# Kernel tuning notes

Hardware: AMD Instinct MI355X
Metric: run time of the kernel (lower is better)

The kernel has to match this reference:

```python
import jax, jax.numpy as jnp
import numpy as np

T, B, E, H = 512, 128, 512, 512
MEM, CTX = 500, 300

def setup_inputs() -> dict:
    key = jax.random.key(0)
    ks = jax.random.split(key, 16)
    s = 0.05
    return {
        "input_seqs": jax.random.normal(ks[0], (B, T, E), jnp.float32),
        "input_lengths": jax.random.randint(ks[1], (B,), 1, T + 1),
        "Wih_f": jax.random.normal(ks[2], (4 * H, E + CTX), jnp.float32) * s,
        "Whh_f": jax.random.normal(ks[3], (4 * H, H), jnp.float32) * s,
        "bih_f": jax.random.normal(ks[4], (4 * H,), jnp.float32) * s,
        "bhh_f": jax.random.normal(ks[5], (4 * H,), jnp.float32) * s,
        "Wih_b": jax.random.normal(ks[6], (4 * H, E + CTX), jnp.float32) * s,
        "Whh_b": jax.random.normal(ks[7], (4 * H, H), jnp.float32) * s,
        "bih_b": jax.random.normal(ks[8], (4 * H,), jnp.float32) * s,
        "bhh_b": jax.random.normal(ks[9], (4 * H,), jnp.float32) * s,
        "Mk_f": jax.random.normal(ks[10], (MEM, H), jnp.float32) * s,
        "Mv_f": jax.random.normal(ks[11], (CTX, MEM), jnp.float32) * s,
        "Mk_b": jax.random.normal(ks[12], (MEM, H), jnp.float32) * s,
        "Mv_b": jax.random.normal(ks[13], (CTX, MEM), jnp.float32) * s,
    }

def _mem_ctx(h, Mk, Mv):
    # exp-key softmax read: exp(h Mk^T) normalized by row sum, then project to CTX
    a = jnp.exp(h @ Mk.T)                      # [B, MEM]
    return (a / jnp.sum(a, axis=-1, keepdims=True)) @ Mv.T  # [B, CTX]

def _cell(x, h, c, Wih, Whh, b):
    g = x @ Wih.T + h @ Whh.T + b              # [B, 4H], gate order i,f,g,o
    i, f, gg, o = jnp.split(g, 4, axis=-1)
    c = jax.nn.sigmoid(f) * c + jax.nn.sigmoid(i) * jnp.tanh(gg)
    return jax.nn.sigmoid(o) * jnp.tanh(c), c

def reference(input_seqs, input_lengths, Wih_f, Whh_f, bih_f, bhh_f,
              Wih_b, Whh_b, bih_b, bhh_b, Mk_f, Mv_f, Mk_b, Mv_b):
    xs = jnp.transpose(input_seqs, (1, 0, 2))          # [T, B, E]
    dt = xs.dtype
    mask = (jnp.arange(T)[:, None] < input_lengths[None, :]).astype(dt)[:, :, None]  # [T,B,1]
    b_f = bih_f + bhh_f
    b_b = bih_b + bhh_b
    z = jnp.zeros((B, H), dt)
    zf = jnp.zeros((), dt)
    one = jnp.ones((), dt)

    def fstep(carry, x):
        h, c, flag = carry
        ctx = flag * _mem_ctx(h, Mk_f, Mv_f)           # step 0 uses zero dummy context
        h, c = _cell(jnp.concatenate([x, ctx], -1), h, c, Wih_f, Whh_f, b_f)
        return (h, c, one), h
    _, f_hs = jax.lax.scan(fstep, (z, z, zf), xs)      # [T, B, H] per-step hidden

    def bstep(carry, xm):
        x, m = xm
        hm, h, c, flag = carry
        ctx = flag * _mem_ctx(hm, Mk_b, Mv_b)
        h, c = _cell(jnp.concatenate([x, ctx], -1), h, c, Wih_b, Whh_b, b_b)
        return (h * m, h, c, one), None                # masked hidden feeds next memory read
    (h_b, _, _, _), _ = jax.lax.scan(bstep, (z, z, z, zf), (xs[::-1], mask[::-1]))

    idx = jnp.clip(input_lengths - 1, 0, T - 1)
    h_f = f_hs[idx, jnp.arange(B)]                     # final valid forward hidden per example
    # permute(1,2,0).view(B,-1): interleave fwd/bwd per hidden unit
    return jnp.stack([h_f, h_b], axis=-1).reshape(B, 2 * H)
```

## Files before the change

### kernel.cpp

```cpp
#include <hip/hip_runtime.h>
#include <hip/hip_bf16.h>

#define T_   512
#define B_   128
#define E_   512
#define H_   512
#define G4_  2048
#define MEM_ 500
#define CTX_ 300
#define EC_  (E_ + CTX_)
#define SPIN_MAX 65536

typedef short sh8  __attribute__((ext_vector_type(8)));
typedef float f32x4 __attribute__((ext_vector_type(4)));

struct ScanParams {
  const float* __restrict__ x;
  const short* __restrict__ xbf;
  const int*   __restrict__ len;
  const float* __restrict__ Wih0; const float* __restrict__ Whh0;
  const float* __restrict__ bih0; const float* __restrict__ bhh0;
  const float* __restrict__ Wih1; const float* __restrict__ Whh1;
  const float* __restrict__ bih1; const float* __restrict__ bhh1;
  const float* __restrict__ Mk0;  const float* __restrict__ Mk1;
  const float* __restrict__ Mf;
  short* __restrict__ hbf;
  short* __restrict__ aB;
  unsigned* __restrict__ bar;
  float* __restrict__ out;
};

__device__ __forceinline__ float sigm_(float x) { return 1.f / (1.f + __expf(-x)); }
__device__ __forceinline__ float tanh_(float x) { return 1.f - 2.f / (__expf(2.f * x) + 1.f); }
__device__ __forceinline__ short f2bs(float f) {
  __hip_bfloat16 h = __float2bfloat16(f);
  short s; __builtin_memcpy(&s, &h, 2); return s;
}
__device__ __forceinline__ float bs2f(short s) {
  unsigned u = ((unsigned)(unsigned short)s) << 16;
  float f; __builtin_memcpy(&f, &u, 4); return f;
}

struct F16 { sh8 v[16]; };
__device__ __forceinline__ void gld16(F16& f, const short* base) {
  asm volatile(
      "global_load_dwordx4 %0, %16, off sc1\n\t"
      "global_load_dwordx4 %1, %16, off offset:64 sc1\n\t"
      "global_load_dwordx4 %2, %16, off offset:128 sc1\n\t"
      "global_load_dwordx4 %3, %16, off offset:192 sc1\n\t"
      "global_load_dwordx4 %4, %16, off offset:256 sc1\n\t"
      "global_load_dwordx4 %5, %16, off offset:320 sc1\n\t"
      "global_load_dwordx4 %6, %16, off offset:384 sc1\n\t"
      "global_load_dwordx4 %7, %16, off offset:448 sc1\n\t"
      "global_load_dwordx4 %8, %16, off offset:512 sc1\n\t"
      "global_load_dwordx4 %9, %16, off offset:576 sc1\n\t"
      "global_load_dwordx4 %10, %16, off offset:640 sc1\n\t"
      "global_load_dwordx4 %11, %16, off offset:704 sc1\n\t"
      "global_load_dwordx4 %12, %16, off offset:768 sc1\n\t"
      "global_load_dwordx4 %13, %16, off offset:832 sc1\n\t"
      "global_load_dwordx4 %14, %16, off offset:896 sc1\n\t"
      "global_load_dwordx4 %15, %16, off offset:960 sc1\n\t"
      "s_waitcnt vmcnt(0)"
      : "=&v"(f.v[0]), "=&v"(f.v[1]), "=&v"(f.v[2]), "=&v"(f.v[3]),
        "=&v"(f.v[4]), "=&v"(f.v[5]), "=&v"(f.v[6]), "=&v"(f.v[7]),
        "=&v"(f.v[8]), "=&v"(f.v[9]), "=&v"(f.v[10]), "=&v"(f.v[11]),
        "=&v"(f.v[12]), "=&v"(f.v[13]), "=&v"(f.v[14]), "=&v"(f.v[15])
      : "v"(base)
      : "memory");
}

__device__ __forceinline__ void st4s(short* base, unsigned d0, unsigned d1,
                                     unsigned d2, unsigned d3) {
  asm volatile(
      "global_store_short %4, %0, off sc1\n\t"
      "global_store_short %4, %1, off offset:1024 sc1\n\t"
      "global_store_short %4, %2, off offset:2048 sc1\n\t"
      "global_store_short %4, %3, off offset:3072 sc1\n\t"
      "s_waitcnt vmcnt(0)"
      :: "v"(d0), "v"(d1), "v"(d2), "v"(d3), "v"(base) : "memory");
}

__device__ __forceinline__ void st8s(short* base, const unsigned* d) {
  asm volatile(
      "global_store_short %8, %0, off sc1\n\t"
      "global_store_short %8, %1, off offset:1024 sc1\n\t"
      "global_store_short %8, %2, off offset:2048 sc1\n\t"
      "global_store_short %8, %3, off offset:3072 sc1\n\t"
      "global_store_short %8, %4, off offset:8 sc1\n\t"
      "global_store_short %8, %5, off offset:1032 sc1\n\t"
      "global_store_short %8, %6, off offset:2056 sc1\n\t"
      "global_store_short %8, %7, off offset:3080 sc1"
      :: "v"(d[0]), "v"(d[1]), "v"(d[2]), "v"(d[3]),
         "v"(d[4]), "v"(d[5]), "v"(d[6]), "v"(d[7]), "v"(base) : "memory");
}

__device__ __forceinline__ bool hchk(const unsigned* hflW, unsigned ep, int lane) {
  unsigned v = __hip_atomic_load(&hflW[lane], __ATOMIC_RELAXED, __HIP_MEMORY_SCOPE_AGENT);
  return __all((int)(v >= ep));
}
__device__ __forceinline__ bool achk(const unsigned* aflW, unsigned ep, int lane) {
  unsigned v = __hip_atomic_load(&aflW[lane & 31], __ATOMIC_RELAXED, __HIP_MEMORY_SCOPE_AGENT);
  return __all((int)(v >= ep));
}
__device__ __forceinline__ void spin_h(const unsigned* hflW, unsigned ep, int lane) {
  int n = 0;
  while (!hchk(hflW, ep, lane) && n < SPIN_MAX) { __builtin_amdgcn_s_sleep(1); ++n; }
}
__device__ __forceinline__ void spin_a(const unsigned* aflW, unsigned ep, int lane) {
  int n = 0;
  while (!achk(aflW, ep, lane) && n < SPIN_MAX) { __builtin_amdgcn_s_sleep(1); ++n; }
}
__device__ __forceinline__ void fset(unsigned* slot, unsigned ep, int lane) {
  if (lane == 0)
    __hip_atomic_store(slot, ep, __ATOMIC_RELAXED, __HIP_MEMORY_SCOPE_AGENT);
}

__global__ __launch_bounds__(256) void xcvt_kernel(const float* __restrict__ x,
                                                   short* __restrict__ xbf) {
  const size_t i = ((size_t)blockIdx.x * 256 + threadIdx.x) * 8;
  f32x4 a = *reinterpret_cast<const f32x4*>(x + i);
  f32x4 b = *reinterpret_cast<const f32x4*>(x + i + 4);
  sh8 v;
  #pragma unroll
  for (int j = 0; j < 4; ++j) { v[j] = f2bs(a[j]); v[4 + j] = f2bs(b[j]); }
  *reinterpret_cast<sh8*>(xbf + i) = v;
}

__global__ __launch_bounds__(256) void mfused_kernel(
    const float* __restrict__ WihF, const float* __restrict__ WihB,
    const float* __restrict__ MvF,  const float* __restrict__ MvB,
    float* __restrict__ Mf) {
  const int d  = blockIdx.x >> 7;
  const int j0 = (blockIdx.x & 127) * 16;
  const float* __restrict__ Wih = d ? WihB : WihF;
  const float* __restrict__ Mv  = d ? MvB  : MvF;
  __shared__ float Wl[16][CTX_ + 1];
  for (int i = threadIdx.x; i < 16 * CTX_; i += 256) {
    int r = i / CTX_, cc = i - r * CTX_;
    Wl[r][cc] = Wih[(size_t)(j0 + r) * EC_ + E_ + cc];
  }
  __syncthreads();
  const int jj = threadIdx.x & 15;
  for (int m = threadIdx.x >> 4; m < MEM_; m += 16) {
    float acc = 0.f;
    for (int cc = 0; cc < CTX_; ++cc)
      acc = fmaf(Mv[cc * MEM_ + m], Wl[jj][cc], acc);
    Mf[(size_t)d * MEM_ * G4_ + (size_t)m * G4_ + j0 + jj] = acc;
  }
}

__global__ __launch_bounds__(512, 1) void scan_kernel(ScanParams p) {
  const int dir  = blockIdx.x >> 6;
  const int w    = blockIdx.x & 63;
  const int tid  = threadIdx.x;
  const int wv   = tid >> 6;
  const int lane = tid & 63;

  __shared__ __align__(16) short WgL[32 * 2 * 64 * 8];
  __shared__ __align__(16) short MkL[16 * 64 * 8];
  __shared__ __align__(16) short MfL[16 * 2 * 64 * 8];
  __shared__ int LvL[B_];

  const float* __restrict__ Wihd = dir ? p.Wih1 : p.Wih0;
  const float* __restrict__ Whhd = dir ? p.Whh1 : p.Whh0;
  const float* __restrict__ bihd = dir ? p.bih1 : p.bih0;
  const float* __restrict__ bhhd = dir ? p.bhh1 : p.bhh0;
  const float* __restrict__ Mkd  = dir ? p.Mk1  : p.Mk0;
  const float* __restrict__ Mfd  = p.Mf + (size_t)dir * MEM_ * G4_;
  short* __restrict__ aBd = p.aB + (size_t)dir * B_ * 512;

  unsigned* __restrict__ hflW = p.bar + (size_t)(dir * 8 + wv) * 64;
  unsigned* __restrict__ aflW = p.bar + 1024 + (size_t)(dir * 8 + wv) * 32;

  const bool prod = ((w & 1) == dir);
  const int  ct   = w >> 1;

  for (int i = tid; i < 32 * 2 * 64; i += 512) {
    const int ks = i >> 7, r2 = i & 127, ct2 = r2 >> 6, l2 = r2 & 63;
    const int col = l2 & 15, kg = l2 >> 4;
    const int k0 = ks * 32 + kg * 8;
    const int gc = (col & 3) * H_ + 8 * w + 4 * ct2 + (col >> 2);
    const float* src = (k0 < E_) ? (Wihd + (size_t)gc * EC_ + k0)
                                 : (Whhd + (size_t)gc * H_ + (k0 - E_));
    sh8 v;
    #pragma unroll
    for (int j = 0; j < 8; ++j) v[j] = f2bs(src[j]);
    *reinterpret_cast<sh8*>(&WgL[i * 8]) = v;
  }
  for (int i = tid; i < 16 * 64; i += 512) {
    const int ks = i >> 6, l2 = i & 63;
    const int col = l2 & 15, kg = l2 >> 4;
    const int k0 = ks * 32 + kg * 8;
    const int mr = 16 * ct + col;
    sh8 v;
    #pragma unroll
    for (int j = 0; j < 8; ++j)
      v[j] = (mr < MEM_) ? f2bs(Mkd[(size_t)mr * H_ + k0 + j]) : (short)0;
    *reinterpret_cast<sh8*>(&MkL[i * 8]) = v;
  }
  for (int i = tid; i < 16 * 2 * 64; i += 512) {
    const int ks = i >> 7, r2 = i & 127, ct2 = r2 >> 6, l2 = r2 & 63;
    const int col = l2 & 15, kg = l2 >> 4;
    const int gc = (col & 3) * H_ + 8 * w + 4 * ct2 + (col >> 2);
    const int m0 = ks * 32 + kg * 8;
    sh8 v;
    #pragma unroll
    for (int j = 0; j < 8; ++j)
      v[j] = (m0 + j < MEM_) ? f2bs(Mfd[(size_t)(m0 + j) * G4_ + gc]) : (short)0;
    *reinterpret_cast<sh8*>(&MfL[i * 8]) = v;
  }
  if (tid < B_) LvL[tid] = p.len[tid];

  const int cc  = lane & 15;
  const int q   = cc & 3;
  const int uu  = cc >> 2;
  const int kg8 = (lane >> 4) * 8;
  const int arow = lane & 15;
  float biasl[2];
  #pragma unroll
  for (int ct2 = 0; ct2 < 2; ++ct2) {
    const int gc = q * H_ + 8 * w + 4 * ct2 + uu;
    biasl[ct2] = bihd[gc] + bhhd[gc];
  }

  float creg[2][4] = {{0.f,0.f,0.f,0.f},{0.f,0.f,0.f,0.f}};
  __syncthreads();

  const int mylen = LvL[16 * wv + arow];

  auto xhalf = [&](int t, f32x4* acc) {
    if (p.xbf) {
      const short* xb = p.xbf + ((size_t)(16 * wv + arow) * T_ + t) * E_ + kg8;
      for (int ks = 0; ks < 16; ++ks) {
        sh8 af = *reinterpret_cast<const sh8*>(xb + ks * 32);
        acc[0] = __builtin_amdgcn_mfma_f32_16x16x32_bf16(
            af, *reinterpret_cast<const sh8*>(&WgL[((ks * 2 + 0) * 64 + lane) * 8]), acc[0], 0, 0, 0);
        acc[1] = __builtin_amdgcn_mfma_f32_16x16x32_bf16(
            af, *reinterpret_cast<const sh8*>(&WgL[((ks * 2 + 1) * 64 + lane) * 8]), acc[1], 0, 0, 0);
      }
    } else {
      const float* xp0 = p.x + ((size_t)(16 * wv + arow) * T_ + t) * E_ + kg8;
      for (int ks = 0; ks < 16; ++ks) {
        f32x4 v0 = *reinterpret_cast<const f32x4*>(xp0 + ks * 32);
        f32x4 v1 = *reinterpret_cast<const f32x4*>(xp0 + ks * 32 + 4);
        sh8 af;
        #pragma unroll
        for (int j = 0; j < 4; ++j) { af[j] = f2bs(v0[j]); af[4 + j] = f2bs(v1[j]); }
        acc[0] = __builtin_amdgcn_mfma_f32_16x16x32_bf16(
            af, *reinterpret_cast<const sh8*>(&WgL[((ks * 2 + 0) * 64 + lane) * 8]), acc[0], 0, 0, 0);
        acc[1] = __builtin_amdgcn_mfma_f32_16x16x32_bf16(
            af, *reinterpret_cast<const sh8*>(&WgL[((ks * 2 + 1) * 64 + lane) * 8]), acc[1], 0, 0, 0);
      }
    }
  };

  f32x4 accX[2] = {(f32x4){0,0,0,0}, (f32x4){0,0,0,0}};
  xhalf(dir ? T_ - 1 : 0, accX);

  for (int s = 0; s < T_; ++s) {
    const int t   = dir ? (T_ - 1 - s) : s;
    const int cur = s & 1, prv = cur ^ 1;
    const short* __restrict__ hb_prev = p.hbf + ((size_t)(prv * 2 + dir)) * B_ * H_;
    short*       __restrict__ hb_cur  = p.hbf + ((size_t)(cur * 2 + dir)) * B_ * H_;

    const short* hrow = hb_prev + (size_t)(16 * wv + arow) * H_ + kg8;

    f32x4 accG[2] = { accX[0], accX[1] };

    if (s > 0) spin_h(hflW, (unsigned)s, lane);
    __builtin_amdgcn_sched_barrier(0);
    F16 fH;
    gld16(fH, hrow);

    if (prod) {
      f32x4 accA = (f32x4){0, 0, 0, 0};
      if (dir) {
        const sh8 z8 = (sh8){0,0,0,0,0,0,0,0};
        const bool keep = (t + 1) < mylen;
        for (int ks = 0; ks < 16; ++ks) {
          sh8 af = keep ? fH.v[ks] : z8;
          accA = __builtin_amdgcn_mfma_f32_16x16x32_bf16(
              af, *reinterpret_cast<const sh8*>(&MkL[(ks * 64 + lane) * 8]), accA, 0, 0, 0);
        }
      } else {
        for (int ks = 0; ks < 16; ++ks)
          accA = __builtin_amdgcn_mfma_f32_16x16x32_bf16(
              fH.v[ks], *reinterpret_cast<const sh8*>(&MkL[(ks * 64 + lane) * 8]), accA, 0, 0, 0);
      }
      const int m = 16 * ct + arow;
      unsigned d[4];
      #pragma unroll
      for (int r = 0; r < 4; ++r) {
        float e = (m < MEM_) ? __expf(accA[r]) : 0.f;
        d[r] = (unsigned)(unsigned short)f2bs(e);
      }
      st4s(aBd + (size_t)(16 * wv + 4 * (lane >> 4)) * 512 + m, d[0], d[1], d[2], d[3]);
      fset(&aflW[ct], (unsigned)(s + 1), lane);
    }

    for (int ks = 0; ks < 16; ++ks) {
      accG[0] = __builtin_amdgcn_mfma_f32_16x16x32_bf16(
          fH.v[ks], *reinterpret_cast<const sh8*>(&WgL[(((16 + ks) * 2 + 0) * 64 + lane) * 8]), accG[0], 0, 0, 0);
      accG[1] = __builtin_amdgcn_mfma_f32_16x16x32_bf16(
          fH.v[ks], *reinterpret_cast<const sh8*>(&WgL[(((16 + ks) * 2 + 1) * 64 + lane) * 8]), accG[1], 0, 0, 0);
    }

    accX[0] = (f32x4){0,0,0,0}; accX[1] = (f32x4){0,0,0,0};
    if (s + 1 < T_) xhalf(dir ? (T_ - 2 - s) : (s + 1), accX);

    f32x4 accC[2] = {(f32x4){0,0,0,0}, (f32x4){0,0,0,0}};
    float inv4[4] = {0.f, 0.f, 0.f, 0.f};
    if (s > 0) {
      spin_a(aflW, (unsigned)(s + 1), lane);
      __builtin_amdgcn_sched_barrier(0);
      F16 fC;
      gld16(fC, aBd + (size_t)(16 * wv + arow) * 512 + kg8);
      float rs = 0.f;
      for (int ks = 0; ks < 16; ++ks) {
        accC[0] = __builtin_amdgcn_mfma_f32_16x16x32_bf16(
            fC.v[ks], *reinterpret_cast<const sh8*>(&MfL[((ks * 2 + 0) * 64 + lane) * 8]), accC[0], 0, 0, 0);
        accC[1] = __builtin_amdgcn_mfma_f32_16x16x32_bf16(
            fC.v[ks], *reinterpret_cast<const sh8*>(&MfL[((ks * 2 + 1) * 64 + lane) * 8]), accC[1], 0, 0, 0);
        #pragma unroll
        for (int j = 0; j < 8; ++j) rs += bs2f(fC.v[ks][j]);
      }
      rs += __shfl_xor(rs, 16);
      rs += __shfl_xor(rs, 32);
      #pragma unroll
      for (int r = 0; r < 4; ++r)
        inv4[r] = 1.f / __shfl(rs, 4 * (lane >> 4) + r);
    }

    unsigned hsd[8]; float hvv[2][4];
    #pragma unroll
    for (int ct2 = 0; ct2 < 2; ++ct2) {
      float g4[4];
      #pragma unroll
      for (int r = 0; r < 4; ++r) {
        float v = accG[ct2][r] + biasl[ct2];
        if (s > 0) v += accC[ct2][r] * inv4[r];
        g4[r] = v;
      }
      #pragma unroll
      for (int r = 0; r < 4; ++r) {
        const float x1 = __shfl_xor(g4[r], 1);
        const float x2 = __shfl_xor(g4[r], 2);
        const float x3 = __shfl_xor(g4[r], 3);
        const float iv = (q==0)?g4[r]:(q==1)?x1:(q==2)?x2:x3;
        const float fv = (q==0)?x1:(q==1)?g4[r]:(q==2)?x3:x2;
        const float gv = (q==0)?x2:(q==1)?x3:(q==2)?g4[r]:x1;
        const float ov = (q==0)?x3:(q==1)?x2:(q==2)?x1:g4[r];
        float cv = creg[ct2][r];
        cv = sigm_(fv) * cv + sigm_(iv) * tanh_(gv);
        const float hv = sigm_(ov) * tanh_(cv);
        creg[ct2][r] = cv;
        hvv[ct2][r] = hv;
        hsd[ct2 * 4 + r] = (unsigned)(unsigned short)f2bs(hv);
      }
    }
    if (q == 0) {
      const int b0 = 16 * wv + 4 * (lane >> 4);
      const int unit0 = 8 * w + uu;
      unsigned hord[8] = {hsd[0],hsd[1],hsd[2],hsd[3],hsd[4],hsd[5],hsd[6],hsd[7]};
      st8s(hb_cur + (size_t)b0 * H_ + unit0, hord);
      #pragma unroll
      for (int ct2 = 0; ct2 < 2; ++ct2) {
        #pragma unroll
        for (int r = 0; r < 4; ++r) {
          const int b = b0 + r;
          const int unit = unit0 + 4 * ct2;
          if (dir == 0) {
            if (t == LvL[b] - 1) p.out[b * (2 * H_) + 2 * unit] = hvv[ct2][r];
          } else {
            if (s == T_ - 1) p.out[b * (2 * H_) + 2 * unit + 1] = hvv[ct2][r];
          }
        }
      }
    }
    asm volatile("s_waitcnt vmcnt(0)" ::: "memory");
    fset(&hflW[w], (unsigned)(s + 1), lane);
  }
}

extern "C" void kernel_launch(void* const* d_in, const int* in_sizes, int n_in,
                              void* d_out, int out_size, void* d_ws, size_t ws_size,
                              hipStream_t stream) {
  (void)in_sizes; (void)n_in; (void)out_size;

  ScanParams p;
  p.x    = (const float*)d_in[0];
  p.len  = (const int*)  d_in[1];
  p.Wih0 = (const float*)d_in[2];
  p.Whh0 = (const float*)d_in[3];
  p.bih0 = (const float*)d_in[4];
  p.bhh0 = (const float*)d_in[5];
  p.Wih1 = (const float*)d_in[6];
  p.Whh1 = (const float*)d_in[7];
  p.bih1 = (const float*)d_in[8];
  p.bhh1 = (const float*)d_in[9];
  p.Mk0  = (const float*)d_in[10];
  const float* MvF = (const float*)d_in[11];
  p.Mk1  = (const float*)d_in[12];
  const float* MvB = (const float*)d_in[13];

  char* ws = (char*)d_ws;
  size_t off = 0;
  auto alloc = [&](size_t bytes) -> void* {
    void* ptr = ws + off; off += (bytes + 255) & ~(size_t)255; return ptr;
  };
  float*    Mf   = (float*)   alloc((size_t)2 * MEM_ * G4_ * 4);
  short*    hbf  = (short*)   alloc((size_t)2 * 2 * B_ * H_ * 2);
  short*    aB   = (short*)   alloc((size_t)2 * B_ * 512 * 2);
  unsigned* bar  = (unsigned*)alloc((size_t)1536 * sizeof(unsigned));
  size_t xbf_off = off;
  short*    xbf  = (short*)   alloc((size_t)B_ * T_ * E_ * 2);
  const bool useXbf = (ws_size >= xbf_off + (size_t)B_ * T_ * E_ * 2);

  p.Mf = Mf; p.hbf = hbf; p.aB = aB; p.bar = bar;
  p.xbf = useXbf ? xbf : nullptr;
  p.out = (float*)d_out;

  hipMemsetAsync(hbf, 0, (size_t)2 * 2 * B_ * H_ * 2, stream);
  hipMemsetAsync(bar, 0, (size_t)1536 * sizeof(unsigned), stream);

  if (useXbf) {
    const size_t n8 = (size_t)B_ * T_ * E_ / 8;
    xcvt_kernel<<<dim3((unsigned)(n8 / 256)), dim3(256), 0, stream>>>(p.x, xbf);
  }
  mfused_kernel<<<dim3(256), dim3(256), 0, stream>>>(
      (const float*)d_in[2], (const float*)d_in[6], MvF, MvB, Mf);

  void* args[] = { &p };
  hipLaunchCooperativeKernel((const void*)scan_kernel, dim3(128), dim3(512),
                             args, 0, stream);
}
```

Before: 9.811 ms.

## Compute memory-attention redundantly per block to drop cross-block attention exchange

Each block now computes the full exp(h·Mk^T) attention for its own batch rows, reading pre-fragmented bf16 Mk from a new global buffer, and feeds the scores through a small LDS scratch straight into the context MFMA. This replaces the producer/consumer split, where half the blocks wrote attention scores to global memory and the others spin-waited on flags. The intent is to remove one inter-block synchronization and round trip per timestep. In exchange every block does 32x more Mk MFMA work and streams Mk from L2 each step. The next-step x projection is also moved after the h flag set so it overlaps with other blocks' waiting.

New measurement: 21.26 ms. +116.7%, slower.

```diff
diff --git a/kernel.cpp b/kernel.cpp
--- a/kernel.cpp
+++ b/kernel.cpp
@@ -17,6 +17,7 @@
 struct ScanParams {
   const float* __restrict__ x;
   const short* __restrict__ xbf;
+  const short* __restrict__ mkf;
   const int*   __restrict__ len;
   const float* __restrict__ Wih0; const float* __restrict__ Whh0;
   const float* __restrict__ bih0; const float* __restrict__ bhh0;
@@ -25,7 +26,6 @@
   const float* __restrict__ Mk0;  const float* __restrict__ Mk1;
   const float* __restrict__ Mf;
   short* __restrict__ hbf;
-  short* __restrict__ aB;
   unsigned* __restrict__ bar;
   float* __restrict__ out;
 };
@@ -35,10 +35,6 @@
 __device__ __forceinline__ short f2bs(float f) {
   __hip_bfloat16 h = __float2bfloat16(f);
   short s; __builtin_memcpy(&s, &h, 2); return s;
-}
-__device__ __forceinline__ float bs2f(short s) {
-  unsigned u = ((unsigned)(unsigned short)s) << 16;
-  float f; __builtin_memcpy(&f, &u, 4); return f;
 }
 
 struct F16 { sh8 v[16]; };
@@ -69,17 +65,6 @@
       : "memory");
 }
 
-__device__ __forceinline__ void st4s(short* base, unsigned d0, unsigned d1,
-                                     unsigned d2, unsigned d3) {
-  asm volatile(
-      "global_store_short %4, %0, off sc1\n\t"
-      "global_store_short %4, %1, off offset:1024 sc1\n\t"
-      "global_store_short %4, %2, off offset:2048 sc1\n\t"
-      "global_store_short %4, %3, off offset:3072 sc1\n\t"
-      "s_waitcnt vmcnt(0)"
-      :: "v"(d0), "v"(d1), "v"(d2), "v"(d3), "v"(base) : "memory");
-}
-
 __device__ __forceinline__ void st8s(short* base, const unsigned* d) {
   asm volatile(
       "global_store_short %8, %0, off sc1\n\t"
@@ -98,17 +83,9 @@
   unsigned v = __hip_atomic_load(&hflW[lane], __ATOMIC_RELAXED, __HIP_MEMORY_SCOPE_AGENT);
   return __all((int)(v >= ep));
 }
-__device__ __forceinline__ bool achk(const unsigned* aflW, unsigned ep, int lane) {
-  unsigned v = __hip_atomic_load(&aflW[lane & 31], __ATOMIC_RELAXED, __HIP_MEMORY_SCOPE_AGENT);
-  return __all((int)(v >= ep));
-}
 __device__ __forceinline__ void spin_h(const unsigned* hflW, unsigned ep, int lane) {
   int n = 0;
   while (!hchk(hflW, ep, lane) && n < SPIN_MAX) { __builtin_amdgcn_s_sleep(1); ++n; }
-}
-__device__ __forceinline__ void spin_a(const unsigned* aflW, unsigned ep, int lane) {
-  int n = 0;
-  while (!achk(aflW, ep, lane) && n < SPIN_MAX) { __builtin_amdgcn_s_sleep(1); ++n; }
 }
 __device__ __forceinline__ void fset(unsigned* slot, unsigned ep, int lane) {
   if (lane == 0)
@@ -124,6 +101,24 @@
   #pragma unroll
   for (int j = 0; j < 4; ++j) { v[j] = f2bs(a[j]); v[4 + j] = f2bs(b[j]); }
   *reinterpret_cast<sh8*>(xbf + i) = v;
+}
+
+__global__ __launch_bounds__(256) void mkfrag_kernel(const float* __restrict__ Mk0,
+                                                     const float* __restrict__ Mk1,
+                                                     short* __restrict__ mkf) {
+  int s = blockIdx.x * 256 + threadIdx.x;
+  const int lane = s & 63; int t = s >> 6;
+  const int ks = t & 15; t >>= 4;
+  const int mt = t & 31; t >>= 5;
+  const int d  = t;
+  const float* __restrict__ Mk = d ? Mk1 : Mk0;
+  const int m  = 16 * mt + (lane & 15);
+  const int k0 = 32 * ks + (lane >> 4) * 8;
+  sh8 v;
+  #pragma unroll
+  for (int j = 0; j < 8; ++j)
+    v[j] = (m < MEM_) ? f2bs(Mk[(size_t)m * H_ + k0 + j]) : (short)0;
+  *reinterpret_cast<sh8*>(&mkf[(size_t)s * 8]) = v;
 }
 
 __global__ __launch_bounds__(256) void mfused_kernel(
@@ -157,23 +152,18 @@
   const int lane = tid & 63;
 
   __shared__ __align__(16) short WgL[32 * 2 * 64 * 8];
-  __shared__ __align__(16) short MkL[16 * 64 * 8];
   __shared__ __align__(16) short MfL[16 * 2 * 64 * 8];
+  __shared__ __align__(16) short aScr[8][16][40];
   __shared__ int LvL[B_];
 
   const float* __restrict__ Wihd = dir ? p.Wih1 : p.Wih0;
   const float* __restrict__ Whhd = dir ? p.Whh1 : p.Whh0;
   const float* __restrict__ bihd = dir ? p.bih1 : p.bih0;
   const float* __restrict__ bhhd = dir ? p.bhh1 : p.bhh0;
-  const float* __restrict__ Mkd  = dir ? p.Mk1  : p.Mk0;
   const float* __restrict__ Mfd  = p.Mf + (size_t)dir * MEM_ * G4_;
-  short* __restrict__ aBd = p.aB + (size_t)dir * B_ * 512;
+  const short* __restrict__ mkfd = p.mkf + (size_t)dir * 32 * 16 * 64 * 8;
 
   unsigned* __restrict__ hflW = p.bar + (size_t)(dir * 8 + wv) * 64;
-  unsigned* __restrict__ aflW = p.bar + 1024 + (size_t)(dir * 8 + wv) * 32;
-
-  const bool prod = ((w & 1) == dir);
-  const int  ct   = w >> 1;
 
   for (int i = tid; i < 32 * 2 * 64; i += 512) {
     const int ks = i >> 7, r2 = i & 127, ct2 = r2 >> 6, l2 = r2 & 63;
@@ -186,17 +176,6 @@
     #pragma unroll
     for (int j = 0; j < 8; ++j) v[j] = f2bs(src[j]);
     *reinterpret_cast<sh8*>(&WgL[i * 8]) = v;
-  }
-  for (int i = tid; i < 16 * 64; i += 512) {
-    const int ks = i >> 6, l2 = i & 63;
-    const int col = l2 & 15, kg = l2 >> 4;
-    const int k0 = ks * 32 + kg * 8;
-    const int mr = 16 * ct + col;
-    sh8 v;
-    #pragma unroll
-    for (int j = 0; j < 8; ++j)
-      v[j] = (mr < MEM_) ? f2bs(Mkd[(size_t)mr * H_ + k0 + j]) : (short)0;
-    *reinterpret_cast<sh8*>(&MkL[i * 8]) = v;
   }
   for (int i = tid; i < 16 * 2 * 64; i += 512) {
     const int ks = i >> 7, r2 = i & 127, ct2 = r2 >> 6, l2 = r2 & 63;
@@ -272,32 +251,6 @@
     F16 fH;
     gld16(fH, hrow);
 
-    if (prod) {
-      f32x4 accA = (f32x4){0, 0, 0, 0};
-      if (dir) {
-        const sh8 z8 = (sh8){0,0,0,0,0,0,0,0};
-        const bool keep = (t + 1) < mylen;
-        for (int ks = 0; ks < 16; ++ks) {
-          sh8 af = keep ? fH.v[ks] : z8;
-          accA = __builtin_amdgcn_mfma_f32_16x16x32_bf16(
-              af, *reinterpret_cast<const sh8*>(&MkL[(ks * 64 + lane) * 8]), accA, 0, 0, 0);
-        }
-      } else {
-        for (int ks = 0; ks < 16; ++ks)
-          accA = __builtin_amdgcn_mfma_f32_16x16x32_bf16(
-              fH.v[ks], *reinterpret_cast<const sh8*>(&MkL[(ks * 64 + lane) * 8]), accA, 0, 0, 0);
-      }
-      const int m = 16 * ct + arow;
-      unsigned d[4];
-      #pragma unroll
-      for (int r = 0; r < 4; ++r) {
-        float e = (m < MEM_) ? __expf(accA[r]) : 0.f;
-        d[r] = (unsigned)(unsigned short)f2bs(e);
-      }
-      st4s(aBd + (size_t)(16 * wv + 4 * (lane >> 4)) * 512 + m, d[0], d[1], d[2], d[3]);
-      fset(&aflW[ct], (unsigned)(s + 1), lane);
-    }
-
     for (int ks = 0; ks < 16; ++ks) {
       accG[0] = __builtin_amdgcn_mfma_f32_16x16x32_bf16(
           fH.v[ks], *reinterpret_cast<const sh8*>(&WgL[(((16 + ks) * 2 + 0) * 64 + lane) * 8]), accG[0], 0, 0, 0);
@@ -305,30 +258,48 @@
           fH.v[ks], *reinterpret_cast<const sh8*>(&WgL[(((16 + ks) * 2 + 1) * 64 + lane) * 8]), accG[1], 0, 0, 0);
     }
 
-    accX[0] = (f32x4){0,0,0,0}; accX[1] = (f32x4){0,0,0,0};
-    if (s + 1 < T_) xhalf(dir ? (T_ - 2 - s) : (s + 1), accX);
-
     f32x4 accC[2] = {(f32x4){0,0,0,0}, (f32x4){0,0,0,0}};
     float inv4[4] = {0.f, 0.f, 0.f, 0.f};
     if (s > 0) {
-      spin_a(aflW, (unsigned)(s + 1), lane);
-      __builtin_amdgcn_sched_barrier(0);
-      F16 fC;
-      gld16(fC, aBd + (size_t)(16 * wv + arow) * 512 + kg8);
-      float rs = 0.f;
-      for (int ks = 0; ks < 16; ++ks) {
+      float rsl[4] = {0.f, 0.f, 0.f, 0.f};
+      const sh8 z8 = (sh8){0,0,0,0,0,0,0,0};
+      const bool keep = !dir || ((t + 1) < mylen);
+      short* as = &aScr[wv][0][0];
+      for (int mtp = 0; mtp < 16; ++mtp) {
+        const short* mkb = mkfd + (size_t)(2 * mtp) * 8192 + lane * 8;
+        f32x4 aA0 = (f32x4){0,0,0,0}, aA1 = (f32x4){0,0,0,0};
+        for (int ks = 0; ks < 16; ++ks) {
+          sh8 af = keep ? fH.v[ks] : z8;
+          sh8 b0 = *reinterpret_cast<const sh8*>(mkb + ks * 512);
+          sh8 b1 = *reinterpret_cast<const sh8*>(mkb + 8192 + ks * 512);
+          aA0 = __builtin_amdgcn_mfma_f32_16x16x32_bf16(af, b0, aA0, 0, 0, 0);
+          aA1 = __builtin_amdgcn_mfma_f32_16x16x32_bf16(af, b1, aA1, 0, 0, 0);
+        }
+        const int m0 = 32 * mtp + (lane & 15);
+        const int m1 = m0 + 16;
+        #pragma unroll
+        for (int r = 0; r < 4; ++r) {
+          float e0 = (m0 < MEM_) ? __expf(aA0[r]) : 0.f;
+          float e1 = (m1 < MEM_) ? __expf(aA1[r]) : 0.f;
+          rsl[r] += e0 + e1;
+          const int row = 4 * (lane >> 4) + r;
+          as[row * 40 + (lane & 15)]      = f2bs(e0);
+          as[row * 40 + 16 + (lane & 15)] = f2bs(e1);
+        }
+        sh8 afr = *reinterpret_cast<const sh8*>(&as[(lane & 15) * 40 + kg8]);
         accC[0] = __builtin_amdgcn_mfma_f32_16x16x32_bf16(
-            fC.v[ks], *reinterpret_cast<const sh8*>(&MfL[((ks * 2 + 0) * 64 + lane) * 8]), accC[0], 0, 0, 0);
+            afr, *reinterpret_cast<const sh8*>(&MfL[((mtp * 2 + 0) * 64 + lane) * 8]), accC[0], 0, 0, 0);
         accC[1] = __builtin_amdgcn_mfma_f32_16x16x32_bf16(
-            fC.v[ks], *reinterpret_cast<const sh8*>(&MfL[((ks * 2 + 1) * 64 + lane) * 8]), accC[1], 0, 0, 0);
-        #pragma unroll
-        for (int j = 0; j < 8; ++j) rs += bs2f(fC.v[ks][j]);
-      }
-      rs += __shfl_xor(rs, 16);
-      rs += __shfl_xor(rs, 32);
+            afr, *reinterpret_cast<const sh8*>(&MfL[((mtp * 2 + 1) * 64 + lane) * 8]), accC[1], 0, 0, 0);
+      }
       #pragma unroll
-      for (int r = 0; r < 4; ++r)
-        inv4[r] = 1.f / __shfl(rs, 4 * (lane >> 4) + r);
+      for (int r = 0; r < 4; ++r) {
+        rsl[r] += __shfl_xor(rsl[r], 1);
+        rsl[r] += __shfl_xor(rsl[r], 2);
+        rsl[r] += __shfl_xor(rsl[r], 4);
+        rsl[r] += __shfl_xor(rsl[r], 8);
+        inv4[r] = 1.f / rsl[r];
+      }
     }
 
     unsigned hsd[8]; float hvv[2][4];
@@ -379,6 +350,9 @@
     }
     asm volatile("s_waitcnt vmcnt(0)" ::: "memory");
     fset(&hflW[w], (unsigned)(s + 1), lane);
+
+    accX[0] = (f32x4){0,0,0,0}; accX[1] = (f32x4){0,0,0,0};
+    if (s + 1 < T_) xhalf(dir ? (T_ - 2 - s) : (s + 1), accX);
   }
 }
 
@@ -410,23 +384,24 @@
   };
   float*    Mf   = (float*)   alloc((size_t)2 * MEM_ * G4_ * 4);
   short*    hbf  = (short*)   alloc((size_t)2 * 2 * B_ * H_ * 2);
-  short*    aB   = (short*)   alloc((size_t)2 * B_ * 512 * 2);
-  unsigned* bar  = (unsigned*)alloc((size_t)1536 * sizeof(unsigned));
+  short*    mkf  = (short*)   alloc((size_t)2 * 32 * 16 * 64 * 8 * 2);
+  unsigned* bar  = (unsigned*)alloc((size_t)1024 * sizeof(unsigned));
   size_t xbf_off = off;
   short*    xbf  = (short*)   alloc((size_t)B_ * T_ * E_ * 2);
   const bool useXbf = (ws_size >= xbf_off + (size_t)B_ * T_ * E_ * 2);
 
-  p.Mf = Mf; p.hbf = hbf; p.aB = aB; p.bar = bar;
+  p.Mf = Mf; p.hbf = hbf; p.mkf = mkf; p.bar = bar;
   p.xbf = useXbf ? xbf : nullptr;
   p.out = (float*)d_out;
 
   hipMemsetAsync(hbf, 0, (size_t)2 * 2 * B_ * H_ * 2, stream);
-  hipMemsetAsync(bar, 0, (size_t)1536 * sizeof(unsigned), stream);
+  hipMemsetAsync(bar, 0, (size_t)1024 * sizeof(unsigned), stream);
 
   if (useXbf) {
     const size_t n8 = (size_t)B_ * T_ * E_ / 8;
     xcvt_kernel<<<dim3((unsigned)(n8 / 256)), dim3(256), 0, stream>>>(p.x, xbf);
   }
+  mkfrag_kernel<<<dim3(256), dim3(256), 0, stream>>>(p.Mk0, p.Mk1, mkf);
   mfused_kernel<<<dim3(256), dim3(256), 0, stream>>>(
       (const float*)d_in[2], (const float*)d_in[6], MvF, MvB, Mf);
 
```

## Co-locate both directions in one 1024-thread block and stream x-weights from global

Applied to the files above, without the earlier changes.

The persistent scan kernel now runs 64 blocks of 1024 threads, with the forward and backward directions sharing each block as separate wave groups, instead of 128 blocks of 512 threads. To fit both directions in LDS, only the Whh and fused-memory fragments stay in shared memory. The Wih x-part and Mk fragments are pre-packed into bf16 MFMA layout by new prep kernels and read from global or L2 every step. This halves the number of CUs used and may change how the cross-block flag synchronization contends. The cost is extra global traffic per step and more waves per CU sharing one block's resources.

Result: slower. 24.18 ms (+146.5%).

```diff
diff --git a/kernel.cpp b/kernel.cpp
--- a/kernel.cpp
+++ b/kernel.cpp
@@ -17,6 +17,8 @@
 struct ScanParams {
   const float* __restrict__ x;
   const short* __restrict__ xbf;
+  const short* __restrict__ mkf;
+  const short* __restrict__ wgx;
   const int*   __restrict__ len;
   const float* __restrict__ Wih0; const float* __restrict__ Whh0;
   const float* __restrict__ bih0; const float* __restrict__ bhh0;
@@ -126,6 +128,43 @@
   *reinterpret_cast<sh8*>(xbf + i) = v;
 }
 
+__global__ __launch_bounds__(256) void mkfrag_kernel(const float* __restrict__ Mk0,
+                                                     const float* __restrict__ Mk1,
+                                                     short* __restrict__ mkf) {
+  int s = blockIdx.x * 256 + threadIdx.x;
+  const int lane = s & 63; int t = s >> 6;
+  const int ks = t & 15; t >>= 4;
+  const int mt = t & 31; t >>= 5;
+  const int d  = t;
+  const float* __restrict__ Mk = d ? Mk1 : Mk0;
+  const int m  = 16 * mt + (lane & 15);
+  const int k0 = 32 * ks + (lane >> 4) * 8;
+  sh8 v;
+  #pragma unroll
+  for (int j = 0; j < 8; ++j)
+    v[j] = (m < MEM_) ? f2bs(Mk[(size_t)m * H_ + k0 + j]) : (short)0;
+  *reinterpret_cast<sh8*>(&mkf[(size_t)s * 8]) = v;
+}
+
+__global__ __launch_bounds__(256) void wgxfrag_kernel(const float* __restrict__ WihF,
+                                                      const float* __restrict__ WihB,
+                                                      short* __restrict__ wgx) {
+  int s = blockIdx.x * 256 + threadIdx.x;
+  const int lane = s & 63; int t = s >> 6;
+  const int ct2 = t & 1;  t >>= 1;
+  const int ks  = t & 15; t >>= 4;
+  const int w   = t & 63; t >>= 6;
+  const int d   = t;
+  const float* __restrict__ Wih = d ? WihB : WihF;
+  const int col = lane & 15;
+  const int gc  = (col & 3) * H_ + 8 * w + 4 * ct2 + (col >> 2);
+  const int k0  = 32 * ks + (lane >> 4) * 8;
+  sh8 v;
+  #pragma unroll
+  for (int j = 0; j < 8; ++j) v[j] = f2bs(Wih[(size_t)gc * EC_ + k0 + j]);
+  *reinterpret_cast<sh8*>(&wgx[(size_t)s * 8]) = v;
+}
+
 __global__ __launch_bounds__(256) void mfused_kernel(
     const float* __restrict__ WihF, const float* __restrict__ WihB,
     const float* __restrict__ MvF,  const float* __restrict__ MvB,
@@ -149,25 +188,25 @@
   }
 }
 
-__global__ __launch_bounds__(512, 1) void scan_kernel(ScanParams p) {
-  const int dir  = blockIdx.x >> 6;
-  const int w    = blockIdx.x & 63;
+__global__ __launch_bounds__(1024, 1) void scan_kernel(ScanParams p) {
+  const int w    = blockIdx.x;
   const int tid  = threadIdx.x;
-  const int wv   = tid >> 6;
+  const int wave = tid >> 6;
+  const int dir  = wave >> 3;
+  const int wv   = wave & 7;
   const int lane = tid & 63;
 
-  __shared__ __align__(16) short WgL[32 * 2 * 64 * 8];
-  __shared__ __align__(16) short MkL[16 * 64 * 8];
-  __shared__ __align__(16) short MfL[16 * 2 * 64 * 8];
+  __shared__ __align__(16) short WgHL[2 * 16 * 2 * 64 * 8];
+  __shared__ __align__(16) short MfL2[2 * 16 * 2 * 64 * 8];
   __shared__ int LvL[B_];
 
-  const float* __restrict__ Wihd = dir ? p.Wih1 : p.Wih0;
-  const float* __restrict__ Whhd = dir ? p.Whh1 : p.Whh0;
   const float* __restrict__ bihd = dir ? p.bih1 : p.bih0;
   const float* __restrict__ bhhd = dir ? p.bhh1 : p.bhh0;
-  const float* __restrict__ Mkd  = dir ? p.Mk1  : p.Mk0;
-  const float* __restrict__ Mfd  = p.Mf + (size_t)dir * MEM_ * G4_;
+  const short* __restrict__ mkfd = p.mkf + (size_t)dir * 32 * 16 * 64 * 8;
+  const short* __restrict__ wgxw = p.wgx + (size_t)(dir * 64 + w) * 2048 * 8;
   short* __restrict__ aBd = p.aB + (size_t)dir * B_ * 512;
+  const short* __restrict__ WgL = WgHL + (size_t)dir * 16 * 2 * 64 * 8;
+  const short* __restrict__ MfL = MfL2 + (size_t)dir * 16 * 2 * 64 * 8;
 
   unsigned* __restrict__ hflW = p.bar + (size_t)(dir * 8 + wv) * 64;
   unsigned* __restrict__ aflW = p.bar + 1024 + (size_t)(dir * 8 + wv) * 32;
@@ -175,39 +214,29 @@
   const bool prod = ((w & 1) == dir);
   const int  ct   = w >> 1;
 
-  for (int i = tid; i < 32 * 2 * 64; i += 512) {
-    const int ks = i >> 7, r2 = i & 127, ct2 = r2 >> 6, l2 = r2 & 63;
+  for (int i = tid; i < 2 * 16 * 2 * 64; i += 1024) {
+    const int d2 = i >> 11, r = i & 2047;
+    const int ks = r >> 7, r2 = r & 127, ct2 = r2 >> 6, l2 = r2 & 63;
     const int col = l2 & 15, kg = l2 >> 4;
-    const int k0 = ks * 32 + kg * 8;
     const int gc = (col & 3) * H_ + 8 * w + 4 * ct2 + (col >> 2);
-    const float* src = (k0 < E_) ? (Wihd + (size_t)gc * EC_ + k0)
-                                 : (Whhd + (size_t)gc * H_ + (k0 - E_));
+    const float* Whh2 = d2 ? p.Whh1 : p.Whh0;
     sh8 v;
     #pragma unroll
-    for (int j = 0; j < 8; ++j) v[j] = f2bs(src[j]);
-    *reinterpret_cast<sh8*>(&WgL[i * 8]) = v;
-  }
-  for (int i = tid; i < 16 * 64; i += 512) {
-    const int ks = i >> 6, l2 = i & 63;
+    for (int j = 0; j < 8; ++j) v[j] = f2bs(Whh2[(size_t)gc * H_ + 32 * ks + kg * 8 + j]);
+    *reinterpret_cast<sh8*>(&WgHL[i * 8]) = v;
+  }
+  for (int i = tid; i < 2 * 16 * 2 * 64; i += 1024) {
+    const int d2 = i >> 11, r = i & 2047;
+    const int ks = r >> 7, r2 = r & 127, ct2 = r2 >> 6, l2 = r2 & 63;
     const int col = l2 & 15, kg = l2 >> 4;
-    const int k0 = ks * 32 + kg * 8;
-    const int mr = 16 * ct + col;
+    const int gc = (col & 3) * H_ + 8 * w + 4 * ct2 + (col >> 2);
+    const int m0 = 32 * ks + kg * 8;
+    const float* Mf2 = p.Mf + (size_t)d2 * MEM_ * G4_;
     sh8 v;
     #pragma unroll
     for (int j = 0; j < 8; ++j)
-      v[j] = (mr < MEM_) ? f2bs(Mkd[(size_t)mr * H_ + k0 + j]) : (short)0;
-    *reinterpret_cast<sh8*>(&MkL[i * 8]) = v;
-  }
-  for (int i = tid; i < 16 * 2 * 64; i += 512) {
-    const int ks = i >> 7, r2 = i & 127, ct2 = r2 >> 6, l2 = r2 & 63;
-    const int col = l2 & 15, kg = l2 >> 4;
-    const int gc = (col & 3) * H_ + 8 * w + 4 * ct2 + (col >> 2);
-    const int m0 = ks * 32 + kg * 8;
-    sh8 v;
-    #pragma unroll
-    for (int j = 0; j < 8; ++j)
-      v[j] = (m0 + j < MEM_) ? f2bs(Mfd[(size_t)(m0 + j) * G4_ + gc]) : (short)0;
-    *reinterpret_cast<sh8*>(&MfL[i * 8]) = v;
+      v[j] = (m0 + j < MEM_) ? f2bs(Mf2[(size_t)(m0 + j) * G4_ + gc]) : (short)0;
+    *reinterpret_cast<sh8*>(&MfL2[i * 8]) = v;
   }
   if (tid < B_) LvL[tid] = p.len[tid];
 
@@ -233,10 +262,10 @@
       const short* xb = p.xbf + ((size_t)(16 * wv + arow) * T_ + t) * E_ + kg8;
       for (int ks = 0; ks < 16; ++ks) {
         sh8 af = *reinterpret_cast<const sh8*>(xb + ks * 32);
-        acc[0] = __builtin_amdgcn_mfma_f32_16x16x32_bf16(
-            af, *reinterpret_cast<const sh8*>(&WgL[((ks * 2 + 0) * 64 + lane) * 8]), acc[0], 0, 0, 0);
-        acc[1] = __builtin_amdgcn_mfma_f32_16x16x32_bf16(
-            af, *reinterpret_cast<const sh8*>(&WgL[((ks * 2 + 1) * 64 + lane) * 8]), acc[1], 0, 0, 0);
+        sh8 b0 = *reinterpret_cast<const sh8*>(wgxw + ((ks * 2 + 0) * 64 + lane) * 8);
+        sh8 b1 = *reinterpret_cast<const sh8*>(wgxw + ((ks * 2 + 1) * 64 + lane) * 8);
+        acc[0] = __builtin_amdgcn_mfma_f32_16x16x32_bf16(af, b0, acc[0], 0, 0, 0);
+        acc[1] = __builtin_amdgcn_mfma_f32_16x16x32_bf16(af, b1, acc[1], 0, 0, 0);
       }
     } else {
       const float* xp0 = p.x + ((size_t)(16 * wv + arow) * T_ + t) * E_ + kg8;
@@ -246,10 +275,10 @@
         sh8 af;
         #pragma unroll
         for (int j = 0; j < 4; ++j) { af[j] = f2bs(v0[j]); af[4 + j] = f2bs(v1[j]); }
-        acc[0] = __builtin_amdgcn_mfma_f32_16x16x32_bf16(
-            af, *reinterpret_cast<const sh8*>(&WgL[((ks * 2 + 0) * 64 + lane) * 8]), acc[0], 0, 0, 0);
-        acc[1] = __builtin_amdgcn_mfma_f32_16x16x32_bf16(
-            af, *reinterpret_cast<const sh8*>(&WgL[((ks * 2 + 1) * 64 + lane) * 8]), acc[1], 0, 0, 0);
+        sh8 b0 = *reinterpret_cast<const sh8*>(wgxw + ((ks * 2 + 0) * 64 + lane) * 8);
+        sh8 b1 = *reinterpret_cast<const sh8*>(wgxw + ((ks * 2 + 1) * 64 + lane) * 8);
+        acc[0] = __builtin_amdgcn_mfma_f32_16x16x32_bf16(af, b0, acc[0], 0, 0, 0);
+        acc[1] = __builtin_amdgcn_mfma_f32_16x16x32_bf16(af, b1, acc[1], 0, 0, 0);
       }
     }
   };
@@ -274,18 +303,13 @@
 
     if (prod) {
       f32x4 accA = (f32x4){0, 0, 0, 0};
-      if (dir) {
-        const sh8 z8 = (sh8){0,0,0,0,0,0,0,0};
-        const bool keep = (t + 1) < mylen;
-        for (int ks = 0; ks < 16; ++ks) {
-          sh8 af = keep ? fH.v[ks] : z8;
-          accA = __builtin_amdgcn_mfma_f32_16x16x32_bf16(
-              af, *reinterpret_cast<const sh8*>(&MkL[(ks * 64 + lane) * 8]), accA, 0, 0, 0);
-        }
-      } else {
-        for (int ks = 0; ks < 16; ++ks)
-          accA = __builtin_amdgcn_mfma_f32_16x16x32_bf16(
-              fH.v[ks], *reinterpret_cast<const sh8*>(&MkL[(ks * 64 + lane) * 8]), accA, 0, 0, 0);
+      const sh8 z8 = (sh8){0,0,0,0,0,0,0,0};
+      const bool keep = !dir || ((t + 1) < mylen);
+      for (int ks = 0; ks < 16; ++ks) {
+        sh8 af = keep ? fH.v[ks] : z8;
+        sh8 bf = *reinterpret_cast<const sh8*>(
+            mkfd + ((size_t)ct * 16 + ks) * 512 + lane * 8);
+        accA = __builtin_amdgcn_mfma_f32_16x16x32_bf16(af, bf, accA, 0, 0, 0);
       }
       const int m = 16 * ct + arow;
       unsigned d[4];
@@ -300,9 +324,9 @@
 
     for (int ks = 0; ks < 16; ++ks) {
       accG[0] = __builtin_amdgcn_mfma_f32_16x16x32_bf16(
-          fH.v[ks], *reinterpret_cast<const sh8*>(&WgL[(((16 + ks) * 2 + 0) * 64 + lane) * 8]), accG[0], 0, 0, 0);
+          fH.v[ks], *reinterpret_cast<const sh8*>(&WgL[((ks * 2 + 0) * 64 + lane) * 8]), accG[0], 0, 0, 0);
       accG[1] = __builtin_amdgcn_mfma_f32_16x16x32_bf16(
-          fH.v[ks], *reinterpret_cast<const sh8*>(&WgL[(((16 + ks) * 2 + 1) * 64 + lane) * 8]), accG[1], 0, 0, 0);
+          fH.v[ks], *reinterpret_cast<const sh8*>(&WgL[((ks * 2 + 1) * 64 + lane) * 8]), accG[1], 0, 0, 0);
     }
 
     accX[0] = (f32x4){0,0,0,0}; accX[1] = (f32x4){0,0,0,0};
@@ -411,12 +435,14 @@
   float*    Mf   = (float*)   alloc((size_t)2 * MEM_ * G4_ * 4);
   short*    hbf  = (short*)   alloc((size_t)2 * 2 * B_ * H_ * 2);
   short*    aB   = (short*)   alloc((size_t)2 * B_ * 512 * 2);
+  short*    mkf  = (short*)   alloc((size_t)2 * 32 * 16 * 64 * 8 * 2);
+  short*    wgx  = (short*)   alloc((size_t)262144 * 8 * 2);
   unsigned* bar  = (unsigned*)alloc((size_t)1536 * sizeof(unsigned));
   size_t xbf_off = off;
   short*    xbf  = (short*)   alloc((size_t)B_ * T_ * E_ * 2);
   const bool useXbf = (ws_size >= xbf_off + (size_t)B_ * T_ * E_ * 2);
 
-  p.Mf = Mf; p.hbf = hbf; p.aB = aB; p.bar = bar;
+  p.Mf = Mf; p.hbf = hbf; p.aB = aB; p.mkf = mkf; p.wgx = wgx; p.bar = bar;
   p.xbf = useXbf ? xbf : nullptr;
   p.out = (float*)d_out;
 
@@ -427,10 +453,13 @@
     const size_t n8 = (size_t)B_ * T_ * E_ / 8;
     xcvt_kernel<<<dim3((unsigned)(n8 / 256)), dim3(256), 0, stream>>>(p.x, xbf);
   }
+  mkfrag_kernel<<<dim3(256), dim3(256), 0, stream>>>(p.Mk0, p.Mk1, mkf);
+  wgxfrag_kernel<<<dim3(1024), dim3(256), 0, stream>>>(
+      (const float*)d_in[2], (const float*)d_in[6], wgx);
   mfused_kernel<<<dim3(256), dim3(256), 0, stream>>>(
       (const float*)d_in[2], (const float*)d_in[6], MvF, MvB, Mf);
 
   void* args[] = { &p };
-  hipLaunchCooperativeKernel((const void*)scan_kernel, dim3(128), dim3(512),
+  hipLaunchCooperativeKernel((const void*)scan_kernel, dim3(64), dim3(1024),
                              args, 0, stream);
 }
```
